# Kernel optimization log

Measured on AMD Instinct MI355X. Metric: run time of the kernel, lower is better.

Reference implementation:

```python
import jax, jax.numpy as jnp
import numpy as np

B, N, C, K1, CO = 8, 1024, 64, 3, 64  # K1 = K+1


def _prelu(x, a):
    return jnp.where(x >= 0, x, a * x)


def setup_inputs() -> dict:
    key = jax.random.key(0)
    ks = jax.random.split(key, 12)
    X_real = jax.random.normal(ks[0], (B, N, C), jnp.float32)
    X_imag = jax.random.normal(ks[1], (B, N, C), jnp.float32)
    # complex laplacian polynomial stack (B, K+1, N, N), scaled like a normalized laplacian
    L_real = jax.random.normal(ks[2], (B, K1, N, N), jnp.float32) * 0.03
    L_imag = jax.random.normal(ks[3], (B, K1, N, N), jnp.float32) * 0.03
    # Chebyshev complex weights: uniform(-stdv, stdv) then normalized to unit magnitude
    stdv = 1.0 / np.sqrt(CO)
    wr = jax.random.uniform(ks[4], (K1, C, CO), jnp.float32, -stdv, stdv)
    wi = jax.random.uniform(ks[5], (K1, C, CO), jnp.float32, -stdv, stdv)
    mag = jnp.sqrt(wr ** 2 + wi ** 2)
    w_real, w_imag = wr / mag, wi / mag
    # CVLinear(2C, 1): complex weight split into src (X_i) and dst (X_j) halves
    astd = 1.0 / np.sqrt(2 * C)
    a_src_r = jax.random.uniform(ks[6], (C,), jnp.float32, -astd, astd)
    a_src_i = jax.random.uniform(ks[7], (C,), jnp.float32, -astd, astd)
    a_dst_r = jax.random.uniform(ks[8], (C,), jnp.float32, -astd, astd)
    a_dst_i = jax.random.uniform(ks[9], (C,), jnp.float32, -astd, astd)
    attn_b_r = jax.random.uniform(ks[10], (), jnp.float32, -astd, astd)
    attn_b_i = jax.random.uniform(ks[11], (), jnp.float32, -astd, astd)
    alpha_r = jnp.float32(0.25)  # CPReLU slopes
    alpha_i = jnp.float32(0.25)
    return dict(X_real=X_real, X_imag=X_imag, L_real=L_real, L_imag=L_imag,
                a_src_r=a_src_r, a_src_i=a_src_i, a_dst_r=a_dst_r, a_dst_i=a_dst_i,
                attn_b_r=attn_b_r, attn_b_i=attn_b_i, alpha_r=alpha_r, alpha_i=alpha_i,
                w_real=w_real, w_imag=w_imag)


def reference(X_real, X_imag, L_real, L_imag, a_src_r, a_src_i, a_dst_r, a_dst_i,
              attn_b_r, attn_b_i, alpha_r, alpha_i, w_real, w_imag):
    # --- attention: complex linear over [X_i ; X_j], decomposed GAT-style ---
    # (z @ a) for complex z, a: real = zr@ar - zi@ai ; imag = zr@ai + zi@ar
    si_r = X_real @ a_src_r - X_imag @ a_src_i  # (B, N)
    si_i = X_real @ a_src_i + X_imag @ a_src_r
    sj_r = X_real @ a_dst_r - X_imag @ a_dst_i
    sj_i = X_real @ a_dst_i + X_imag @ a_dst_r
    s_r = si_r[:, :, None] + sj_r[:, None, :] + attn_b_r  # (B, N, N) scores[b,i,j]
    s_i = si_i[:, :, None] + sj_i[:, None, :] + attn_b_i
    # CPReLU: PReLU on real and imag parts independently
    s_r = _prelu(s_r, alpha_r)
    s_i = _prelu(s_i, alpha_i)
    # PhaseSoftMax(dim=1): softmax over magnitudes along axis 1, keep phase
    mag = jnp.sqrt(s_r ** 2 + s_i ** 2)
    scale = jax.nn.softmax(mag, axis=1) / jnp.maximum(mag, 1e-12)
    a_r, a_i = scale * s_r, scale * s_i  # complex attn weights (B, N, N)
    # modulate complex laplacian: L * attn (broadcast over K dim)
    Lm_r = L_real * a_r[:, None] - L_imag * a_i[:, None]  # (B, K+1, N, N)
    Lm_i = L_real * a_i[:, None] + L_imag * a_r[:, None]
    # --- Chebyshev sum: sum_k (L_k X) W_k, complex ---
    LX_r = jnp.einsum('bknm,bmc->bknc', Lm_r, X_real) - jnp.einsum('bknm,bmc->bknc', Lm_i, X_imag)
    LX_i = jnp.einsum('bknm,bmc->bknc', Lm_r, X_imag) + jnp.einsum('bknm,bmc->bknc', Lm_i, X_real)
    out_r = jnp.einsum('bknc,kco->bno', LX_r, w_real) - jnp.einsum('bknc,kco->bno', LX_i, w_imag)
    out_i = jnp.einsum('bknc,kco->bno', LX_r, w_imag) + jnp.einsum('bknc,kco->bno', LX_i, w_real)
    return jnp.stack([out_r, out_i])  # (2, B, N, C_out)
```

## Files before the change

kernel.cpp:

```cpp
#include <hip/hip_runtime.h>

typedef __attribute__((ext_vector_type(8))) short bf16x8;
typedef __attribute__((ext_vector_type(4))) float f32x4;
typedef unsigned int uint32;
typedef unsigned short u16;

#define BN 1024

__device__ __align__(16) float g_stats[6 * 8192];
__device__ __align__(16) u16   g_Xt[8 * 16 * 2 * 64 * 64];
__device__ __align__(16) u16   g_wt[6 * 64 * 192];
__device__ __align__(16) float g_part[2048 * 6144];

__device__ __forceinline__ u16 f2bf(float x) {
    uint32 u = __float_as_uint(x);
    u += 0x7fffu + ((u >> 16) & 1u);
    return (u16)(u >> 16);
}
__device__ __forceinline__ float bf2f(u16 h) {
    return __uint_as_float(((uint32)h) << 16);
}

__global__ void k_sisj(const float* __restrict__ Xr, const float* __restrict__ Xi,
                       const float* __restrict__ asr, const float* __restrict__ asi,
                       const float* __restrict__ adr, const float* __restrict__ adi) {
    int wid = threadIdx.x >> 6, lane = threadIdx.x & 63;
    int bn = blockIdx.x * 4 + wid;
    float xr = Xr[(size_t)bn * 64 + lane], xi = Xi[(size_t)bn * 64 + lane];
    float r0 = asr[lane], i0 = asi[lane], r1 = adr[lane], i1 = adi[lane];
    float v0 = xr * r0 - xi * i0;
    float v1 = xr * i0 + xi * r0;
    float v2 = xr * r1 - xi * i1;
    float v3 = xr * i1 + xi * r1;
    #pragma unroll
    for (int off = 32; off; off >>= 1) {
        v0 += __shfl_xor(v0, off);
        v1 += __shfl_xor(v1, off);
        v2 += __shfl_xor(v2, off);
        v3 += __shfl_xor(v3, off);
    }
    if (lane == 0) {
        g_stats[bn]         = v0;
        g_stats[8192 + bn]  = v1;
        g_stats[16384 + bn] = v2;
        g_stats[24576 + bn] = v3;
    }
}

__global__ void k_mz(const float* __restrict__ pbr, const float* __restrict__ pbi,
                     const float* __restrict__ par, const float* __restrict__ pai) {
    int wid = threadIdx.x >> 6, lane = threadIdx.x & 63;
    int bj = blockIdx.x * 4 + wid;
    int b = bj >> 10;
    float br = pbr[0], bi = pbi[0], ar = par[0], ai = pai[0];
    float sjrv = g_stats[16384 + bj], sjiv = g_stats[24576 + bj];
    float mags[16];
    float mx = 0.0f;
    #pragma unroll
    for (int t = 0; t < 16; ++t) {
        int i = t * 64 + lane;
        float sr = g_stats[b * BN + i] + sjrv + br;
        float si = g_stats[8192 + b * BN + i] + sjiv + bi;
        sr = sr >= 0.f ? sr : ar * sr;
        si = si >= 0.f ? si : ai * si;
        float m = sqrtf(sr * sr + si * si);
        mags[t] = m;
        mx = fmaxf(mx, m);
    }
    #pragma unroll
    for (int off = 32; off; off >>= 1) mx = fmaxf(mx, __shfl_xor(mx, off));
    float s = 0.f;
    #pragma unroll
    for (int t = 0; t < 16; ++t) s += __expf(mags[t] - mx);
    #pragma unroll
    for (int off = 32; off; off >>= 1) s += __shfl_xor(s, off);
    if (lane == 0) { g_stats[32768 + bj] = mx; g_stats[40960 + bj] = s; }
}

__global__ void k_xt(const float* __restrict__ Xr, const float* __restrict__ Xi) {
    int b = blockIdx.x >> 4, q = blockIdx.x & 15;
    __shared__ float xs[2][64][65];
    int tid = threadIdx.x;
    #pragma unroll 4
    for (int rep = 0; rep < 32; ++rep) {
        int idx = rep * 256 + tid;
        int p = idx >> 12, j = (idx >> 6) & 63, c = idx & 63;
        const float* src = p ? Xi : Xr;
        xs[p][j][c] = src[((size_t)b * BN + q * 64 + j) * 64 + c];
    }
    __syncthreads();
    #pragma unroll
    for (int rep = 0; rep < 4; ++rep) {
        int idx = rep * 256 + tid;
        int p = idx >> 9, c = (idx >> 3) & 63, j8 = idx & 7;
        union { u16 h[8]; uint4 v; } pk;
        #pragma unroll
        for (int jj = 0; jj < 8; ++jj) pk.h[jj] = f2bf(xs[p][j8 * 8 + jj][c]);
        *(uint4*)&g_Xt[(size_t)(((b * 16 + q) * 2 + p) * 64 + c) * 64 + j8 * 8] = pk.v;
    }
}

__global__ void k_wt(const float* __restrict__ wr, const float* __restrict__ wi) {
    int t = blockIdx.x * 256 + threadIdx.x;
    int o = t & 63, kc = t >> 6;
    float vr = wr[t], vi = wi[t];
    u16 rh = f2bf(vr);
    u16 rl = f2bf(vr - bf2f(rh));
    u16 ih = f2bf(vi);
    u16 il = f2bf(vi - bf2f(ih));
    g_wt[(0 * 64 + o) * 192 + kc] = rh;
    g_wt[(1 * 64 + o) * 192 + kc] = rl;
    g_wt[(2 * 64 + o) * 192 + kc] = ih;
    g_wt[(3 * 64 + o) * 192 + kc] = il;
    g_wt[(4 * 64 + o) * 192 + kc] = (u16)(ih ^ 0x8000u);
    g_wt[(5 * 64 + o) * 192 + kc] = (u16)(il ^ 0x8000u);
}

__global__ __launch_bounds__(256) void k_main(
    const float* __restrict__ Lr, const float* __restrict__ Li,
    const float* __restrict__ pbr, const float* __restrict__ pbi,
    const float* __restrict__ par, const float* __restrict__ pai) {
    __shared__ __align__(16) u16 lmS[6912];
    __shared__ __align__(16) float sA[2][16];

    int tid = threadIdx.x, wid = tid >> 6, lane = tid & 63;
    int jh = blockIdx.x & 3, it = (blockIdx.x >> 2) & 63, b = blockIdx.x >> 8;
    int i0 = it * 16;

    const float* sjr_g = g_stats + 16384;
    const float* sji_g = g_stats + 24576;
    const float* Mv_g  = g_stats + 32768;
    const float* Zv_g  = g_stats + 40960;

    if (tid < 32) {
        int p = tid >> 4, i = tid & 15;
        sA[p][i] = g_stats[p * 8192 + b * BN + i0 + i];
    }

    f32x4 zz = {0.f, 0.f, 0.f, 0.f};
    f32x4 accr[3], acci[3];
    #pragma unroll
    for (int k = 0; k < 3; ++k) { accr[k] = zz; acci[k] = zz; }

    float brv = pbr[0], biv = pbi[0], alrv = par[0], aliv = pai[0];

    int ti = tid >> 4, tj4 = tid & 15;
    int arow = lane & 15, kb = (lane >> 4) * 8;

    __syncthreads();
    float sirv = sA[0][ti], siiv = sA[1][ti];

    for (int qi = 0; qi < 4; ++qi) {
        int q = jh * 4 + qi;
        int jj0 = q * 64 + tj4 * 4;
        float4 A = *(const float4*)&sjr_g[b * BN + jj0];
        float4 Bv = *(const float4*)&sji_g[b * BN + jj0];
        float4 C = *(const float4*)&Mv_g[b * BN + jj0];
        float4 D = *(const float4*)&Zv_g[b * BN + jj0];
        float sjr4[4] = {A.x, A.y, A.z, A.w};
        float sji4[4] = {Bv.x, Bv.y, Bv.z, Bv.w};
        float M4[4]   = {C.x, C.y, C.z, C.w};
        float Z4[4]   = {D.x, D.y, D.z, D.w};
        float arj[4], aij[4];
        #pragma unroll
        for (int e = 0; e < 4; ++e) {
            float sr = sirv + sjr4[e] + brv;
            float si = siiv + sji4[e] + biv;
            sr = sr >= 0.f ? sr : alrv * sr;
            si = si >= 0.f ? si : aliv * si;
            float mg = sqrtf(sr * sr + si * si);
            float sc = __expf(mg - M4[e]) / (Z4[e] * fmaxf(mg, 1e-12f));
            arj[e] = sc * sr;
            aij[e] = sc * si;
        }
        #pragma unroll
        for (int k = 0; k < 3; ++k) {
            size_t lbase = ((size_t)(b * 3 + k) * BN + (i0 + ti)) * BN + jj0;
            float4 r4 = *(const float4*)&Lr[lbase];
            float4 s4 = *(const float4*)&Li[lbase];
            float lr4[4] = {r4.x, r4.y, r4.z, r4.w};
            float li4[4] = {s4.x, s4.y, s4.z, s4.w};
            union { u16 h[4]; uint2 v; } pr, pi;
            #pragma unroll
            for (int e = 0; e < 4; ++e) {
                float mr = lr4[e] * arj[e] - li4[e] * aij[e];
                float mi = lr4[e] * aij[e] + li4[e] * arj[e];
                pr.h[e] = f2bf(mr);
                pi.h[e] = f2bf(mi);
            }
            *(uint2*)(lmS + ((k * 2 + 0) * 16 + ti) * 72 + tj4 * 4) = pr.v;
            *(uint2*)(lmS + ((k * 2 + 1) * 16 + ti) * 72 + tj4 * 4) = pi.v;
        }
        bf16x8 Bx[2][2];
        {
            size_t xbase = (size_t)((b * 16 + q) * 2) * 4096 + (wid * 16 + arow) * 64 + kb;
            #pragma unroll
            for (int p = 0; p < 2; ++p)
                #pragma unroll
                for (int ks = 0; ks < 2; ++ks)
                    Bx[p][ks] = *(const bf16x8*)&g_Xt[xbase + p * 4096 + ks * 32];
        }
        __syncthreads();
        #pragma unroll
        for (int k = 0; k < 3; ++k) {
            #pragma unroll
            for (int ks = 0; ks < 2; ++ks) {
                int kc = ks * 32 + kb;
                bf16x8 aR = *(const bf16x8*)(lmS + ((k * 2 + 0) * 16 + arow) * 72 + kc);
                bf16x8 aI = *(const bf16x8*)(lmS + ((k * 2 + 1) * 16 + arow) * 72 + kc);
                bf16x8 aIn;
                #pragma unroll
                for (int z = 0; z < 8; ++z) aIn[z] = (short)(aI[z] ^ (short)0x8000);
                accr[k] = __builtin_amdgcn_mfma_f32_16x16x32_bf16(aR,  Bx[0][ks], accr[k], 0, 0, 0);
                accr[k] = __builtin_amdgcn_mfma_f32_16x16x32_bf16(aIn, Bx[1][ks], accr[k], 0, 0, 0);
                acci[k] = __builtin_amdgcn_mfma_f32_16x16x32_bf16(aR,  Bx[1][ks], acci[k], 0, 0, 0);
                acci[k] = __builtin_amdgcn_mfma_f32_16x16x32_bf16(aI,  Bx[0][ks], acci[k], 0, 0, 0);
            }
        }
        __syncthreads();
    }

    {
        size_t base = (size_t)blockIdx.x * 6144;
        #pragma unroll
        for (int k = 0; k < 3; ++k) {
            #pragma unroll
            for (int p = 0; p < 2; ++p) {
                f32x4 fr = p ? acci[k] : accr[k];
                #pragma unroll
                for (int r = 0; r < 4; ++r) {
                    int row = (lane >> 4) * 4 + r;
                    int kc = k * 64 + wid * 16 + (lane & 15);
                    g_part[base + (size_t)(p * 16 + row) * 192 + kc] = fr[r];
                }
            }
        }
    }
}

__global__ __launch_bounds__(256) void k_out(float* __restrict__ out) {
    __shared__ __align__(16) u16 LXs[12800];
    int tid = threadIdx.x, wid = tid >> 6, lane = tid & 63;
    int b = blockIdx.x >> 6, it = blockIdx.x & 63, i0 = it * 16;
    size_t p0 = (size_t)((b * 64 + it) * 4) * 6144;

    #pragma unroll
    for (int rep = 0; rep < 6; ++rep) {
        int idx = rep * 256 + tid;
        float4 a0 = *(const float4*)&g_part[p0 + (size_t)idx * 4];
        float4 a1 = *(const float4*)&g_part[p0 + 6144 + (size_t)idx * 4];
        float4 a2 = *(const float4*)&g_part[p0 + 12288 + (size_t)idx * 4];
        float4 a3 = *(const float4*)&g_part[p0 + 18432 + (size_t)idx * 4];
        float s[4] = {a0.x + a1.x + a2.x + a3.x, a0.y + a1.y + a2.y + a3.y,
                      a0.z + a1.z + a2.z + a3.z, a0.w + a1.w + a2.w + a3.w};
        int f0 = idx * 4;
        int rc = f0 / 3072, rem = f0 - rc * 3072;
        int row = rem / 192, kc = rem - row * 192;
        #pragma unroll
        for (int t = 0; t < 4; ++t) {
            float v = s[t];
            u16 hi = f2bf(v);
            u16 lo = f2bf(v - bf2f(hi));
            LXs[((rc * 2 + 0) * 16 + row) * 200 + kc + t] = hi;
            LXs[((rc * 2 + 1) * 16 + row) * 200 + kc + t] = lo;
        }
    }
    __syncthreads();

    f32x4 zz = {0.f, 0.f, 0.f, 0.f};
    f32x4 o_r = zz, o_i = zz;
    int arow = lane & 15, kb = (lane >> 4) * 8;
    int o = wid * 16 + arow;
    #pragma unroll
    for (int ks = 0; ks < 6; ++ks) {
        int kc = ks * 32 + kb;
        bf16x8 Arh = *(const bf16x8*)(LXs + (0 * 16 + arow) * 200 + kc);
        bf16x8 Arl = *(const bf16x8*)(LXs + (1 * 16 + arow) * 200 + kc);
        bf16x8 Aih = *(const bf16x8*)(LXs + (2 * 16 + arow) * 200 + kc);
        bf16x8 Ail = *(const bf16x8*)(LXs + (3 * 16 + arow) * 200 + kc);
        bf16x8 Wrh  = *(const bf16x8*)&g_wt[(0 * 64 + o) * 192 + kc];
        bf16x8 Wrl  = *(const bf16x8*)&g_wt[(1 * 64 + o) * 192 + kc];
        bf16x8 Wih  = *(const bf16x8*)&g_wt[(2 * 64 + o) * 192 + kc];
        bf16x8 Wil  = *(const bf16x8*)&g_wt[(3 * 64 + o) * 192 + kc];
        bf16x8 Wihn = *(const bf16x8*)&g_wt[(4 * 64 + o) * 192 + kc];
        bf16x8 Wiln = *(const bf16x8*)&g_wt[(5 * 64 + o) * 192 + kc];
        o_r = __builtin_amdgcn_mfma_f32_16x16x32_bf16(Arh, Wrh,  o_r, 0, 0, 0);
        o_r = __builtin_amdgcn_mfma_f32_16x16x32_bf16(Arh, Wrl,  o_r, 0, 0, 0);
        o_r = __builtin_amdgcn_mfma_f32_16x16x32_bf16(Arl, Wrh,  o_r, 0, 0, 0);
        o_r = __builtin_amdgcn_mfma_f32_16x16x32_bf16(Aih, Wihn, o_r, 0, 0, 0);
        o_r = __builtin_amdgcn_mfma_f32_16x16x32_bf16(Aih, Wiln, o_r, 0, 0, 0);
        o_r = __builtin_amdgcn_mfma_f32_16x16x32_bf16(Ail, Wihn, o_r, 0, 0, 0);
        o_i = __builtin_amdgcn_mfma_f32_16x16x32_bf16(Arh, Wih,  o_i, 0, 0, 0);
        o_i = __builtin_amdgcn_mfma_f32_16x16x32_bf16(Arh, Wil,  o_i, 0, 0, 0);
        o_i = __builtin_amdgcn_mfma_f32_16x16x32_bf16(Arl, Wih,  o_i, 0, 0, 0);
        o_i = __builtin_amdgcn_mfma_f32_16x16x32_bf16(Aih, Wrh,  o_i, 0, 0, 0);
        o_i = __builtin_amdgcn_mfma_f32_16x16x32_bf16(Aih, Wrl,  o_i, 0, 0, 0);
        o_i = __builtin_amdgcn_mfma_f32_16x16x32_bf16(Ail, Wrh,  o_i, 0, 0, 0);
    }
    #pragma unroll
    for (int r = 0; r < 4; ++r) {
        int i = (lane >> 4) * 4 + r;
        size_t off = ((size_t)b * BN + i0 + i) * 64 + o;
        out[off] = o_r[r];
        out[524288 + off] = o_i[r];
    }
}

extern "C" void kernel_launch(void* const* d_in, const int* in_sizes, int n_in,
                              void* d_out, int out_size, void* d_ws, size_t ws_size,
                              hipStream_t stream) {
    const float* Xr  = (const float*)d_in[0];
    const float* Xi  = (const float*)d_in[1];
    const float* Lr  = (const float*)d_in[2];
    const float* Li  = (const float*)d_in[3];
    const float* asr = (const float*)d_in[4];
    const float* asi = (const float*)d_in[5];
    const float* adr = (const float*)d_in[6];
    const float* adi = (const float*)d_in[7];
    const float* pbr = (const float*)d_in[8];
    const float* pbi = (const float*)d_in[9];
    const float* par = (const float*)d_in[10];
    const float* pai = (const float*)d_in[11];
    const float* wr  = (const float*)d_in[12];
    const float* wi  = (const float*)d_in[13];
    float* out = (float*)d_out;

    k_sisj<<<2048, 256, 0, stream>>>(Xr, Xi, asr, asi, adr, adi);
    k_mz<<<2048, 256, 0, stream>>>(pbr, pbi, par, pai);
    k_xt<<<128, 256, 0, stream>>>(Xr, Xi);
    k_wt<<<48, 256, 0, stream>>>(wr, wi);
    k_main<<<2048, 256, 0, stream>>>(Lr, Li, pbr, pbi, par, pai);
    k_out<<<512, 256, 0, stream>>>(out);
}
```

Before: 87.33 us.

## Double k_main row tile to 32 rows and stage column stats in LDS

k_main now handles 32 rows per block instead of 16, which halves the grid and gives each wave two row-group MFMA accumulators. Each block's B-operand X fragments are reused across twice as many rows, and the per-column softmax stats are preloaded once into shared memory instead of being re-read from global memory every iteration. Each thread now loads 8 L elements per row as two float4 loads and writes 16-byte LDS stores. The partial-sum layout and k_out indexing are adjusted to match. In exchange, LDS use and register pressure per block rise and the grid has fewer blocks.

```diff
diff --git a/kernel.cpp b/kernel.cpp
--- a/kernel.cpp
+++ b/kernel.cpp
@@ -10,7 +10,7 @@
 __device__ __align__(16) float g_stats[6 * 8192];
 __device__ __align__(16) u16   g_Xt[8 * 16 * 2 * 64 * 64];
 __device__ __align__(16) u16   g_wt[6 * 64 * 192];
-__device__ __align__(16) float g_part[2048 * 6144];
+__device__ __align__(16) float g_part[1024 * 12288];
 
 __device__ __forceinline__ u16 f2bf(float x) {
     uint32 u = __float_as_uint(x);
@@ -120,31 +120,36 @@
     const float* __restrict__ Lr, const float* __restrict__ Li,
     const float* __restrict__ pbr, const float* __restrict__ pbi,
     const float* __restrict__ par, const float* __restrict__ pai) {
-    __shared__ __align__(16) u16 lmS[6912];
-    __shared__ __align__(16) float sA[2][16];
+    __shared__ __align__(16) u16 lmS[13824];
+    __shared__ __align__(16) float stS[4][256];
+    __shared__ __align__(16) float sA[2][32];
 
     int tid = threadIdx.x, wid = tid >> 6, lane = tid & 63;
-    int jh = blockIdx.x & 3, it = (blockIdx.x >> 2) & 63, b = blockIdx.x >> 8;
-    int i0 = it * 16;
-
-    const float* sjr_g = g_stats + 16384;
-    const float* sji_g = g_stats + 24576;
-    const float* Mv_g  = g_stats + 32768;
-    const float* Zv_g  = g_stats + 40960;
-
-    if (tid < 32) {
-        int p = tid >> 4, i = tid & 15;
-        sA[p][i] = g_stats[p * 8192 + b * BN + i0 + i];
+    int jh = blockIdx.x & 3, it = (blockIdx.x >> 2) & 31, b = blockIdx.x >> 7;
+    int i0 = it * 32;
+
+    {
+        int jg = b * BN + jh * 256 + tid;
+        stS[0][tid] = g_stats[16384 + jg];
+        stS[1][tid] = g_stats[24576 + jg];
+        stS[2][tid] = g_stats[32768 + jg];
+        stS[3][tid] = g_stats[40960 + jg];
+        if (tid < 64) {
+            int p = tid >> 5, i = tid & 31;
+            sA[p][i] = g_stats[p * 8192 + b * BN + i0 + i];
+        }
     }
 
     f32x4 zz = {0.f, 0.f, 0.f, 0.f};
-    f32x4 accr[3], acci[3];
-    #pragma unroll
-    for (int k = 0; k < 3; ++k) { accr[k] = zz; acci[k] = zz; }
+    f32x4 accr[3][2], acci[3][2];
+    #pragma unroll
+    for (int k = 0; k < 3; ++k)
+        #pragma unroll
+        for (int g = 0; g < 2; ++g) { accr[k][g] = zz; acci[k][g] = zz; }
 
     float brv = pbr[0], biv = pbi[0], alrv = par[0], aliv = pai[0];
 
-    int ti = tid >> 4, tj4 = tid & 15;
+    int ti = tid >> 3, tj8 = tid & 7;
     int arow = lane & 15, kb = (lane >> 4) * 8;
 
     __syncthreads();
@@ -152,44 +157,36 @@
 
     for (int qi = 0; qi < 4; ++qi) {
         int q = jh * 4 + qi;
-        int jj0 = q * 64 + tj4 * 4;
-        float4 A = *(const float4*)&sjr_g[b * BN + jj0];
-        float4 Bv = *(const float4*)&sji_g[b * BN + jj0];
-        float4 C = *(const float4*)&Mv_g[b * BN + jj0];
-        float4 D = *(const float4*)&Zv_g[b * BN + jj0];
-        float sjr4[4] = {A.x, A.y, A.z, A.w};
-        float sji4[4] = {Bv.x, Bv.y, Bv.z, Bv.w};
-        float M4[4]   = {C.x, C.y, C.z, C.w};
-        float Z4[4]   = {D.x, D.y, D.z, D.w};
-        float arj[4], aij[4];
-        #pragma unroll
-        for (int e = 0; e < 4; ++e) {
-            float sr = sirv + sjr4[e] + brv;
-            float si = siiv + sji4[e] + biv;
+        int jloc = qi * 64 + tj8 * 8;
+        float arj[8], aij[8];
+        #pragma unroll
+        for (int e = 0; e < 8; ++e) {
+            float sr = sirv + stS[0][jloc + e] + brv;
+            float si = siiv + stS[1][jloc + e] + biv;
             sr = sr >= 0.f ? sr : alrv * sr;
             si = si >= 0.f ? si : aliv * si;
             float mg = sqrtf(sr * sr + si * si);
-            float sc = __expf(mg - M4[e]) / (Z4[e] * fmaxf(mg, 1e-12f));
+            float sc = __expf(mg - stS[2][jloc + e]) / (stS[3][jloc + e] * fmaxf(mg, 1e-12f));
             arj[e] = sc * sr;
             aij[e] = sc * si;
         }
         #pragma unroll
         for (int k = 0; k < 3; ++k) {
-            size_t lbase = ((size_t)(b * 3 + k) * BN + (i0 + ti)) * BN + jj0;
-            float4 r4 = *(const float4*)&Lr[lbase];
-            float4 s4 = *(const float4*)&Li[lbase];
-            float lr4[4] = {r4.x, r4.y, r4.z, r4.w};
-            float li4[4] = {s4.x, s4.y, s4.z, s4.w};
-            union { u16 h[4]; uint2 v; } pr, pi;
+            size_t lbase = ((size_t)(b * 3 + k) * BN + (i0 + ti)) * BN + q * 64 + tj8 * 8;
+            float4 r0 = *(const float4*)&Lr[lbase], r1 = *(const float4*)&Lr[lbase + 4];
+            float4 s0 = *(const float4*)&Li[lbase], s1 = *(const float4*)&Li[lbase + 4];
+            float lr8[8] = {r0.x, r0.y, r0.z, r0.w, r1.x, r1.y, r1.z, r1.w};
+            float li8[8] = {s0.x, s0.y, s0.z, s0.w, s1.x, s1.y, s1.z, s1.w};
+            union { u16 h[8]; uint4 v; } pr, pi;
             #pragma unroll
-            for (int e = 0; e < 4; ++e) {
-                float mr = lr4[e] * arj[e] - li4[e] * aij[e];
-                float mi = lr4[e] * aij[e] + li4[e] * arj[e];
+            for (int e = 0; e < 8; ++e) {
+                float mr = lr8[e] * arj[e] - li8[e] * aij[e];
+                float mi = lr8[e] * aij[e] + li8[e] * arj[e];
                 pr.h[e] = f2bf(mr);
                 pi.h[e] = f2bf(mi);
             }
-            *(uint2*)(lmS + ((k * 2 + 0) * 16 + ti) * 72 + tj4 * 4) = pr.v;
-            *(uint2*)(lmS + ((k * 2 + 1) * 16 + ti) * 72 + tj4 * 4) = pi.v;
+            *(uint4*)(lmS + ((k * 2 + 0) * 32 + ti) * 72 + tj8 * 8) = pr.v;
+            *(uint4*)(lmS + ((k * 2 + 1) * 32 + ti) * 72 + tj8 * 8) = pi.v;
         }
         bf16x8 Bx[2][2];
         {
@@ -206,32 +203,38 @@
             #pragma unroll
             for (int ks = 0; ks < 2; ++ks) {
                 int kc = ks * 32 + kb;
-                bf16x8 aR = *(const bf16x8*)(lmS + ((k * 2 + 0) * 16 + arow) * 72 + kc);
-                bf16x8 aI = *(const bf16x8*)(lmS + ((k * 2 + 1) * 16 + arow) * 72 + kc);
-                bf16x8 aIn;
                 #pragma unroll
-                for (int z = 0; z < 8; ++z) aIn[z] = (short)(aI[z] ^ (short)0x8000);
-                accr[k] = __builtin_amdgcn_mfma_f32_16x16x32_bf16(aR,  Bx[0][ks], accr[k], 0, 0, 0);
-                accr[k] = __builtin_amdgcn_mfma_f32_16x16x32_bf16(aIn, Bx[1][ks], accr[k], 0, 0, 0);
-                acci[k] = __builtin_amdgcn_mfma_f32_16x16x32_bf16(aR,  Bx[1][ks], acci[k], 0, 0, 0);
-                acci[k] = __builtin_amdgcn_mfma_f32_16x16x32_bf16(aI,  Bx[0][ks], acci[k], 0, 0, 0);
+                for (int g = 0; g < 2; ++g) {
+                    bf16x8 aR = *(const bf16x8*)(lmS + ((k * 2 + 0) * 32 + g * 16 + arow) * 72 + kc);
+                    bf16x8 aI = *(const bf16x8*)(lmS + ((k * 2 + 1) * 32 + g * 16 + arow) * 72 + kc);
+                    bf16x8 aIn;
+                    #pragma unroll
+                    for (int z = 0; z < 8; ++z) aIn[z] = (short)(aI[z] ^ (short)0x8000);
+                    accr[k][g] = __builtin_amdgcn_mfma_f32_16x16x32_bf16(aR,  Bx[0][ks], accr[k][g], 0, 0, 0);
+                    accr[k][g] = __builtin_amdgcn_mfma_f32_16x16x32_bf16(aIn, Bx[1][ks], accr[k][g], 0, 0, 0);
+                    acci[k][g] = __builtin_amdgcn_mfma_f32_16x16x32_bf16(aR,  Bx[1][ks], acci[k][g], 0, 0, 0);
+                    acci[k][g] = __builtin_amdgcn_mfma_f32_16x16x32_bf16(aI,  Bx[0][ks], acci[k][g], 0, 0, 0);
+                }
             }
         }
         __syncthreads();
     }
 
     {
-        size_t base = (size_t)blockIdx.x * 6144;
+        size_t base = (size_t)blockIdx.x * 12288;
         #pragma unroll
         for (int k = 0; k < 3; ++k) {
+            int kc = k * 64 + wid * 16 + arow;
             #pragma unroll
-            for (int p = 0; p < 2; ++p) {
-                f32x4 fr = p ? acci[k] : accr[k];
+            for (int g = 0; g < 2; ++g) {
                 #pragma unroll
-                for (int r = 0; r < 4; ++r) {
-                    int row = (lane >> 4) * 4 + r;
-                    int kc = k * 64 + wid * 16 + (lane & 15);
-                    g_part[base + (size_t)(p * 16 + row) * 192 + kc] = fr[r];
+                for (int p = 0; p < 2; ++p) {
+                    f32x4 fr = p ? acci[k][g] : accr[k][g];
+                    #pragma unroll
+                    for (int r = 0; r < 4; ++r) {
+                        int row = g * 16 + (lane >> 4) * 4 + r;
+                        g_part[base + (size_t)(p * 32 + row) * 192 + kc] = fr[r];
+                    }
                 }
             }
         }
@@ -241,21 +244,23 @@
 __global__ __launch_bounds__(256) void k_out(float* __restrict__ out) {
     __shared__ __align__(16) u16 LXs[12800];
     int tid = threadIdx.x, wid = tid >> 6, lane = tid & 63;
-    int b = blockIdx.x >> 6, it = blockIdx.x & 63, i0 = it * 16;
-    size_t p0 = (size_t)((b * 64 + it) * 4) * 6144;
+    int b = blockIdx.x >> 6, it16 = blockIdx.x & 63, i0 = it16 * 16;
+    int it32 = it16 >> 1, rowoff = (it16 & 1) * 16;
+    size_t pb = (size_t)((b * 32 + it32) * 4) * 12288;
 
     #pragma unroll
     for (int rep = 0; rep < 6; ++rep) {
         int idx = rep * 256 + tid;
-        float4 a0 = *(const float4*)&g_part[p0 + (size_t)idx * 4];
-        float4 a1 = *(const float4*)&g_part[p0 + 6144 + (size_t)idx * 4];
-        float4 a2 = *(const float4*)&g_part[p0 + 12288 + (size_t)idx * 4];
-        float4 a3 = *(const float4*)&g_part[p0 + 18432 + (size_t)idx * 4];
-        float s[4] = {a0.x + a1.x + a2.x + a3.x, a0.y + a1.y + a2.y + a3.y,
-                      a0.z + a1.z + a2.z + a3.z, a0.w + a1.w + a2.w + a3.w};
         int f0 = idx * 4;
         int rc = f0 / 3072, rem = f0 - rc * 3072;
         int row = rem / 192, kc = rem - row * 192;
+        size_t off = (size_t)(rc * 32 + rowoff + row) * 192 + kc;
+        float4 a0 = *(const float4*)&g_part[pb + off];
+        float4 a1 = *(const float4*)&g_part[pb + 12288 + off];
+        float4 a2 = *(const float4*)&g_part[pb + 24576 + off];
+        float4 a3 = *(const float4*)&g_part[pb + 36864 + off];
+        float s[4] = {a0.x + a1.x + a2.x + a3.x, a0.y + a1.y + a2.y + a3.y,
+                      a0.z + a1.z + a2.z + a3.z, a0.w + a1.w + a2.w + a3.w};
         #pragma unroll
         for (int t = 0; t < 4; ++t) {
             float v = s[t];
@@ -329,6 +334,6 @@
     k_mz<<<2048, 256, 0, stream>>>(pbr, pbi, par, pai);
     k_xt<<<128, 256, 0, stream>>>(Xr, Xi);
     k_wt<<<48, 256, 0, stream>>>(wr, wi);
-    k_main<<<2048, 256, 0, stream>>>(Lr, Li, pbr, pbi, par, pai);
+    k_main<<<1024, 256, 0, stream>>>(Lr, Li, pbr, pbi, par, pai);
     k_out<<<512, 256, 0, stream>>>(out);
 }
```

After: 98.13 us. 1.12x slower.

## Double-buffer Laplacian tiles via async global-to-LDS loads and halve j-split

Applied to the files above, without the earlier changes.

The main kernel now streams the L_real/L_imag tiles straight into a double-buffered shared-memory region with global_load_lds, prefetching the next 64-column chunk while the current one is processed. Explicit vmcnt waits and raw barriers replace __syncthreads. Per-column softmax stats are cached once in LDS instead of being reloaded each iteration, and each block now covers 512 columns instead of 256. That halves the block count and the partial-sum traffic that k_out must reduce. The trade-off is much higher LDS use per block and lower occupancy and grid parallelism, and the hand-tuned waitcnt values are fragile.

```diff
diff --git a/kernel.cpp b/kernel.cpp
--- a/kernel.cpp
+++ b/kernel.cpp
@@ -10,7 +10,7 @@
 __device__ __align__(16) float g_stats[6 * 8192];
 __device__ __align__(16) u16   g_Xt[8 * 16 * 2 * 64 * 64];
 __device__ __align__(16) u16   g_wt[6 * 64 * 192];
-__device__ __align__(16) float g_part[2048 * 6144];
+__device__ __align__(16) float g_part[1024 * 6144];
 
 __device__ __forceinline__ u16 f2bf(float x) {
     uint32 u = __float_as_uint(x);
@@ -19,6 +19,11 @@
 }
 __device__ __forceinline__ float bf2f(u16 h) {
     return __uint_as_float(((uint32)h) << 16);
+}
+__device__ __forceinline__ void gl_lds16(const float* g, float* l) {
+    __builtin_amdgcn_global_load_lds(
+        (const __attribute__((address_space(1))) uint32*)g,
+        (__attribute__((address_space(3))) uint32*)l, 16, 0, 0);
 }
 
 __global__ void k_sisj(const float* __restrict__ Xr, const float* __restrict__ Xi,
@@ -120,64 +125,95 @@
     const float* __restrict__ Lr, const float* __restrict__ Li,
     const float* __restrict__ pbr, const float* __restrict__ pbi,
     const float* __restrict__ par, const float* __restrict__ pai) {
+    __shared__ __align__(16) float Lbuf[2][6144];
     __shared__ __align__(16) u16 lmS[6912];
+    __shared__ __align__(16) float stS[4][512];
     __shared__ __align__(16) float sA[2][16];
 
-    int tid = threadIdx.x, wid = tid >> 6, lane = tid & 63;
-    int jh = blockIdx.x & 3, it = (blockIdx.x >> 2) & 63, b = blockIdx.x >> 8;
+    int tid = threadIdx.x, w = tid >> 6, lane = tid & 63;
+    int jh = blockIdx.x & 1, it = (blockIdx.x >> 1) & 63, b = blockIdx.x >> 7;
     int i0 = it * 16;
-
-    const float* sjr_g = g_stats + 16384;
-    const float* sji_g = g_stats + 24576;
-    const float* Mv_g  = g_stats + 32768;
-    const float* Zv_g  = g_stats + 40960;
-
-    if (tid < 32) {
-        int p = tid >> 4, i = tid & 15;
-        sA[p][i] = g_stats[p * 8192 + b * BN + i0 + i];
-    }
+    int arow = lane & 15, kb = (lane >> 4) * 8;
+    int ti = tid >> 4, tj4 = tid & 15;
+
+    {
+        int jg = b * BN + jh * 512 + tid;
+        stS[0][tid] = g_stats[16384 + jg];
+        stS[1][tid] = g_stats[24576 + jg];
+        stS[2][tid] = g_stats[32768 + jg];
+        stS[3][tid] = g_stats[40960 + jg];
+        stS[0][tid + 256] = g_stats[16384 + jg + 256];
+        stS[1][tid + 256] = g_stats[24576 + jg + 256];
+        stS[2][tid + 256] = g_stats[32768 + jg + 256];
+        stS[3][tid + 256] = g_stats[40960 + jg + 256];
+        if (tid < 32) {
+            int p = tid >> 4, i = tid & 15;
+            sA[p][i] = g_stats[p * 8192 + b * BN + i0 + i];
+        }
+    }
+    __syncthreads();
+
+    float brv = pbr[0], biv = pbi[0], alrv = par[0], aliv = pai[0];
+    float sirv = sA[0][ti], siiv = sA[1][ti];
 
     f32x4 zz = {0.f, 0.f, 0.f, 0.f};
     f32x4 accr[3], acci[3];
     #pragma unroll
     for (int k = 0; k < 3; ++k) { accr[k] = zz; acci[k] = zz; }
 
-    float brv = pbr[0], biv = pbi[0], alrv = par[0], aliv = pai[0];
-
-    int ti = tid >> 4, tj4 = tid & 15;
-    int arow = lane & 15, kb = (lane >> 4) * 8;
-
-    __syncthreads();
-    float sirv = sA[0][ti], siiv = sA[1][ti];
-
-    for (int qi = 0; qi < 4; ++qi) {
-        int q = jh * 4 + qi;
-        int jj0 = q * 64 + tj4 * 4;
-        float4 A = *(const float4*)&sjr_g[b * BN + jj0];
-        float4 Bv = *(const float4*)&sji_g[b * BN + jj0];
-        float4 C = *(const float4*)&Mv_g[b * BN + jj0];
-        float4 D = *(const float4*)&Zv_g[b * BN + jj0];
-        float sjr4[4] = {A.x, A.y, A.z, A.w};
-        float sji4[4] = {Bv.x, Bv.y, Bv.z, Bv.w};
-        float M4[4]   = {C.x, C.y, C.z, C.w};
-        float Z4[4]   = {D.x, D.y, D.z, D.w};
+    auto stageL = [&](int q, int buf) {
+        #pragma unroll
+        for (int t = 0; t < 6; ++t) {
+            int l = w * 6 + t;
+            int k = l >> 3, rc = (l >> 2) & 1, rg = l & 3;
+            int row = rg * 4 + (lane >> 4), j = (lane & 15) * 4;
+            const float* src = rc ? Li : Lr;
+            const float* g = src + ((size_t)(b * 3 + k) * BN + (i0 + row)) * BN
+                                 + jh * 512 + q * 64 + j;
+            gl_lds16(g, &Lbuf[buf][l * 256]);
+        }
+    };
+
+    stageL(0, 0);
+
+    #pragma unroll
+    for (int qi = 0; qi < 8; ++qi) {
+        int q = jh * 8 + qi;
+        int cur = qi & 1;
+        bf16x8 Bxr[2], Bxi_[2];
+        {
+            size_t xb = (size_t)((b * 16 + q) * 2) * 4096 + (size_t)(w * 16 + arow) * 64 + kb;
+            #pragma unroll
+            for (int ks = 0; ks < 2; ++ks) {
+                Bxr[ks]  = *(const bf16x8*)&g_Xt[xb + ks * 32];
+                Bxi_[ks] = *(const bf16x8*)&g_Xt[xb + 4096 + ks * 32];
+            }
+        }
+        if (qi < 7) stageL(qi + 1, cur ^ 1);
         float arj[4], aij[4];
-        #pragma unroll
-        for (int e = 0; e < 4; ++e) {
-            float sr = sirv + sjr4[e] + brv;
-            float si = siiv + sji4[e] + biv;
-            sr = sr >= 0.f ? sr : alrv * sr;
-            si = si >= 0.f ? si : aliv * si;
-            float mg = sqrtf(sr * sr + si * si);
-            float sc = __expf(mg - M4[e]) / (Z4[e] * fmaxf(mg, 1e-12f));
-            arj[e] = sc * sr;
-            aij[e] = sc * si;
-        }
+        {
+            int jloc = qi * 64 + tj4 * 4;
+            #pragma unroll
+            for (int e = 0; e < 4; ++e) {
+                float sr = sirv + stS[0][jloc + e] + brv;
+                float si = siiv + stS[1][jloc + e] + biv;
+                sr = sr >= 0.f ? sr : alrv * sr;
+                si = si >= 0.f ? si : aliv * si;
+                float mg = sqrtf(sr * sr + si * si);
+                float sc = __expf(mg - stS[2][jloc + e]) / (stS[3][jloc + e] * fmaxf(mg, 1e-12f));
+                arj[e] = sc * sr;
+                aij[e] = sc * si;
+            }
+        }
+        if (qi < 7) { asm volatile("s_waitcnt vmcnt(10)" ::: "memory"); }
+        else        { asm volatile("s_waitcnt vmcnt(4)"  ::: "memory"); }
+        __builtin_amdgcn_s_barrier();
+        __builtin_amdgcn_sched_barrier(0);
         #pragma unroll
         for (int k = 0; k < 3; ++k) {
-            size_t lbase = ((size_t)(b * 3 + k) * BN + (i0 + ti)) * BN + jj0;
-            float4 r4 = *(const float4*)&Lr[lbase];
-            float4 s4 = *(const float4*)&Li[lbase];
+            int base = (k * 8 + (ti >> 2)) * 256 + (ti & 3) * 64 + tj4 * 4;
+            float4 r4 = *(const float4*)&Lbuf[cur][base];
+            float4 s4 = *(const float4*)&Lbuf[cur][base + 1024];
             float lr4[4] = {r4.x, r4.y, r4.z, r4.w};
             float li4[4] = {s4.x, s4.y, s4.z, s4.w};
             union { u16 h[4]; uint2 v; } pr, pi;
@@ -191,16 +227,9 @@
             *(uint2*)(lmS + ((k * 2 + 0) * 16 + ti) * 72 + tj4 * 4) = pr.v;
             *(uint2*)(lmS + ((k * 2 + 1) * 16 + ti) * 72 + tj4 * 4) = pi.v;
         }
-        bf16x8 Bx[2][2];
-        {
-            size_t xbase = (size_t)((b * 16 + q) * 2) * 4096 + (wid * 16 + arow) * 64 + kb;
-            #pragma unroll
-            for (int p = 0; p < 2; ++p)
-                #pragma unroll
-                for (int ks = 0; ks < 2; ++ks)
-                    Bx[p][ks] = *(const bf16x8*)&g_Xt[xbase + p * 4096 + ks * 32];
-        }
-        __syncthreads();
+        asm volatile("s_waitcnt lgkmcnt(0)" ::: "memory");
+        __builtin_amdgcn_s_barrier();
+        __builtin_amdgcn_sched_barrier(0);
         #pragma unroll
         for (int k = 0; k < 3; ++k) {
             #pragma unroll
@@ -211,26 +240,29 @@
                 bf16x8 aIn;
                 #pragma unroll
                 for (int z = 0; z < 8; ++z) aIn[z] = (short)(aI[z] ^ (short)0x8000);
-                accr[k] = __builtin_amdgcn_mfma_f32_16x16x32_bf16(aR,  Bx[0][ks], accr[k], 0, 0, 0);
-                accr[k] = __builtin_amdgcn_mfma_f32_16x16x32_bf16(aIn, Bx[1][ks], accr[k], 0, 0, 0);
-                acci[k] = __builtin_amdgcn_mfma_f32_16x16x32_bf16(aR,  Bx[1][ks], acci[k], 0, 0, 0);
-                acci[k] = __builtin_amdgcn_mfma_f32_16x16x32_bf16(aI,  Bx[0][ks], acci[k], 0, 0, 0);
-            }
-        }
-        __syncthreads();
+                accr[k] = __builtin_amdgcn_mfma_f32_16x16x32_bf16(aR,  Bxr[ks],  accr[k], 0, 0, 0);
+                acci[k] = __builtin_amdgcn_mfma_f32_16x16x32_bf16(aR,  Bxi_[ks], acci[k], 0, 0, 0);
+                acci[k] = __builtin_amdgcn_mfma_f32_16x16x32_bf16(aI,  Bxr[ks],  acci[k], 0, 0, 0);
+                #pragma unroll
+                for (int z = 0; z < 8; ++z) aIn[z] = (short)(aIn[z]);
+                accr[k] = __builtin_amdgcn_mfma_f32_16x16x32_bf16(aIn, Bxi_[ks], accr[k], 0, 0, 0);
+            }
+        }
+        asm volatile("s_waitcnt lgkmcnt(0)" ::: "memory");
+        __builtin_amdgcn_s_barrier();
     }
 
     {
         size_t base = (size_t)blockIdx.x * 6144;
         #pragma unroll
         for (int k = 0; k < 3; ++k) {
+            int kc = k * 64 + w * 16 + arow;
             #pragma unroll
             for (int p = 0; p < 2; ++p) {
                 f32x4 fr = p ? acci[k] : accr[k];
                 #pragma unroll
                 for (int r = 0; r < 4; ++r) {
                     int row = (lane >> 4) * 4 + r;
-                    int kc = k * 64 + wid * 16 + (lane & 15);
                     g_part[base + (size_t)(p * 16 + row) * 192 + kc] = fr[r];
                 }
             }
@@ -242,17 +274,15 @@
     __shared__ __align__(16) u16 LXs[12800];
     int tid = threadIdx.x, wid = tid >> 6, lane = tid & 63;
     int b = blockIdx.x >> 6, it = blockIdx.x & 63, i0 = it * 16;
-    size_t p0 = (size_t)((b * 64 + it) * 4) * 6144;
+    size_t p0 = (size_t)((b * 64 + it) * 2 + 0) * 6144;
+    size_t p1 = p0 + 6144;
 
     #pragma unroll
     for (int rep = 0; rep < 6; ++rep) {
         int idx = rep * 256 + tid;
-        float4 a0 = *(const float4*)&g_part[p0 + (size_t)idx * 4];
-        float4 a1 = *(const float4*)&g_part[p0 + 6144 + (size_t)idx * 4];
-        float4 a2 = *(const float4*)&g_part[p0 + 12288 + (size_t)idx * 4];
-        float4 a3 = *(const float4*)&g_part[p0 + 18432 + (size_t)idx * 4];
-        float s[4] = {a0.x + a1.x + a2.x + a3.x, a0.y + a1.y + a2.y + a3.y,
-                      a0.z + a1.z + a2.z + a3.z, a0.w + a1.w + a2.w + a3.w};
+        float4 a = *(const float4*)&g_part[p0 + (size_t)idx * 4];
+        float4 c = *(const float4*)&g_part[p1 + (size_t)idx * 4];
+        float s[4] = {a.x + c.x, a.y + c.y, a.z + c.z, a.w + c.w};
         int f0 = idx * 4;
         int rc = f0 / 3072, rem = f0 - rc * 3072;
         int row = rem / 192, kc = rem - row * 192;
@@ -329,6 +359,6 @@
     k_mz<<<2048, 256, 0, stream>>>(pbr, pbi, par, pai);
     k_xt<<<128, 256, 0, stream>>>(Xr, Xi);
     k_wt<<<48, 256, 0, stream>>>(wr, wi);
-    k_main<<<2048, 256, 0, stream>>>(Lr, Li, pbr, pbi, par, pai);
+    k_main<<<1024, 256, 0, stream>>>(Lr, Li, pbr, pbi, par, pai);
     k_out<<<512, 256, 0, stream>>>(out);
 }
```

After: 82.23 us. -5.8%, faster.

## Stage full 256-column L tile in LDS once, then run all MFMAs

Applied to the files above, without the earlier changes.

Instead of four iterations that each load a 64-column slice of L, modulate it, sync twice and run MFMAs, the kernel now stages the j-range statistics in shared memory, loads and modulates the whole 16x256 slab for all three k in one phase, and then runs all eight MFMA steps after a single barrier. Each thread now handles 4 rows x 4 columns with coalesced 1KB row reads, and the negation moves from the A operand to the X operand. The aim is fewer barriers and more memory loads in flight, at the cost of much larger LDS use (about 50KB), which may lower occupancy and leaves no overlap between the load and MFMA phases.

```diff
diff --git a/kernel.cpp b/kernel.cpp
--- a/kernel.cpp
+++ b/kernel.cpp
@@ -120,117 +120,118 @@
     const float* __restrict__ Lr, const float* __restrict__ Li,
     const float* __restrict__ pbr, const float* __restrict__ pbi,
     const float* __restrict__ par, const float* __restrict__ pai) {
-    __shared__ __align__(16) u16 lmS[6912];
+    __shared__ __align__(16) u16 lmS[25344];
+    __shared__ __align__(16) float stS[4][256];
     __shared__ __align__(16) float sA[2][16];
 
-    int tid = threadIdx.x, wid = tid >> 6, lane = tid & 63;
+    int tid = threadIdx.x, w = tid >> 6, lane = tid & 63;
     int jh = blockIdx.x & 3, it = (blockIdx.x >> 2) & 63, b = blockIdx.x >> 8;
-    int i0 = it * 16;
-
-    const float* sjr_g = g_stats + 16384;
-    const float* sji_g = g_stats + 24576;
-    const float* Mv_g  = g_stats + 32768;
-    const float* Zv_g  = g_stats + 40960;
-
-    if (tid < 32) {
-        int p = tid >> 4, i = tid & 15;
-        sA[p][i] = g_stats[p * 8192 + b * BN + i0 + i];
-    }
+    int i0 = it * 16, j0 = jh * 256;
+
+    {
+        int jg = b * BN + j0 + tid;
+        stS[0][tid] = g_stats[16384 + jg];
+        stS[1][tid] = g_stats[24576 + jg];
+        stS[2][tid] = g_stats[32768 + jg];
+        stS[3][tid] = g_stats[40960 + jg];
+        if (tid < 32) {
+            int p = tid >> 4, i = tid & 15;
+            sA[p][i] = g_stats[p * 8192 + b * BN + i0 + i];
+        }
+    }
+    __syncthreads();
+
+    float brv = pbr[0], biv = pbi[0], alrv = par[0], aliv = pai[0];
+
+    {
+        float4 s0 = *(const float4*)&stS[0][lane * 4];
+        float4 s1 = *(const float4*)&stS[1][lane * 4];
+        float4 s2 = *(const float4*)&stS[2][lane * 4];
+        float4 s3 = *(const float4*)&stS[3][lane * 4];
+        float sjr4[4] = {s0.x, s0.y, s0.z, s0.w};
+        float sji4[4] = {s1.x, s1.y, s1.z, s1.w};
+        float M4[4]   = {s2.x, s2.y, s2.z, s2.w};
+        float Z4[4]   = {s3.x, s3.y, s3.z, s3.w};
+        float arj[4][4], aij[4][4];
+        #pragma unroll
+        for (int u = 0; u < 4; ++u) {
+            int row = w * 4 + u;
+            float sirv = sA[0][row], siiv = sA[1][row];
+            #pragma unroll
+            for (int e = 0; e < 4; ++e) {
+                float sr = sirv + sjr4[e] + brv;
+                float si = siiv + sji4[e] + biv;
+                sr = sr >= 0.f ? sr : alrv * sr;
+                si = si >= 0.f ? si : aliv * si;
+                float mg = sqrtf(sr * sr + si * si);
+                float sc = __expf(mg - M4[e]) / (Z4[e] * fmaxf(mg, 1e-12f));
+                arj[u][e] = sc * sr;
+                aij[u][e] = sc * si;
+            }
+        }
+        #pragma unroll
+        for (int k = 0; k < 3; ++k) {
+            #pragma unroll
+            for (int u = 0; u < 4; ++u) {
+                int row = w * 4 + u;
+                size_t gb = ((size_t)(b * 3 + k) * BN + (i0 + row)) * BN + j0 + lane * 4;
+                float4 r4 = *(const float4*)&Lr[gb];
+                float4 s4 = *(const float4*)&Li[gb];
+                float lr4[4] = {r4.x, r4.y, r4.z, r4.w};
+                float li4[4] = {s4.x, s4.y, s4.z, s4.w};
+                union { u16 h[4]; uint2 v; } pr, pi;
+                #pragma unroll
+                for (int e = 0; e < 4; ++e) {
+                    float mr = lr4[e] * arj[u][e] - li4[e] * aij[u][e];
+                    float mi = lr4[e] * aij[u][e] + li4[e] * arj[u][e];
+                    pr.h[e] = f2bf(mr);
+                    pi.h[e] = f2bf(mi);
+                }
+                *(uint2*)(lmS + ((k * 2 + 0) * 16 + row) * 264 + lane * 4) = pr.v;
+                *(uint2*)(lmS + ((k * 2 + 1) * 16 + row) * 264 + lane * 4) = pi.v;
+            }
+        }
+    }
+    __syncthreads();
 
     f32x4 zz = {0.f, 0.f, 0.f, 0.f};
     f32x4 accr[3], acci[3];
     #pragma unroll
     for (int k = 0; k < 3; ++k) { accr[k] = zz; acci[k] = zz; }
-
-    float brv = pbr[0], biv = pbi[0], alrv = par[0], aliv = pai[0];
-
-    int ti = tid >> 4, tj4 = tid & 15;
     int arow = lane & 15, kb = (lane >> 4) * 8;
 
-    __syncthreads();
-    float sirv = sA[0][ti], siiv = sA[1][ti];
-
-    for (int qi = 0; qi < 4; ++qi) {
-        int q = jh * 4 + qi;
-        int jj0 = q * 64 + tj4 * 4;
-        float4 A = *(const float4*)&sjr_g[b * BN + jj0];
-        float4 Bv = *(const float4*)&sji_g[b * BN + jj0];
-        float4 C = *(const float4*)&Mv_g[b * BN + jj0];
-        float4 D = *(const float4*)&Zv_g[b * BN + jj0];
-        float sjr4[4] = {A.x, A.y, A.z, A.w};
-        float sji4[4] = {Bv.x, Bv.y, Bv.z, Bv.w};
-        float M4[4]   = {C.x, C.y, C.z, C.w};
-        float Z4[4]   = {D.x, D.y, D.z, D.w};
-        float arj[4], aij[4];
-        #pragma unroll
-        for (int e = 0; e < 4; ++e) {
-            float sr = sirv + sjr4[e] + brv;
-            float si = siiv + sji4[e] + biv;
-            sr = sr >= 0.f ? sr : alrv * sr;
-            si = si >= 0.f ? si : aliv * si;
-            float mg = sqrtf(sr * sr + si * si);
-            float sc = __expf(mg - M4[e]) / (Z4[e] * fmaxf(mg, 1e-12f));
-            arj[e] = sc * sr;
-            aij[e] = sc * si;
-        }
+    #pragma unroll
+    for (int s = 0; s < 8; ++s) {
+        int q = jh * 4 + (s >> 1);
+        int jin = (s & 1) * 32;
+        size_t xb = (size_t)((b * 16 + q) * 2) * 4096 + (size_t)(w * 16 + arow) * 64 + jin + kb;
+        bf16x8 Bxr = *(const bf16x8*)&g_Xt[xb];
+        bf16x8 Bxi = *(const bf16x8*)&g_Xt[xb + 4096];
+        bf16x8 nBxi;
+        #pragma unroll
+        for (int z = 0; z < 8; ++z) nBxi[z] = (short)(Bxi[z] ^ (short)0x8000);
         #pragma unroll
         for (int k = 0; k < 3; ++k) {
-            size_t lbase = ((size_t)(b * 3 + k) * BN + (i0 + ti)) * BN + jj0;
-            float4 r4 = *(const float4*)&Lr[lbase];
-            float4 s4 = *(const float4*)&Li[lbase];
-            float lr4[4] = {r4.x, r4.y, r4.z, r4.w};
-            float li4[4] = {s4.x, s4.y, s4.z, s4.w};
-            union { u16 h[4]; uint2 v; } pr, pi;
-            #pragma unroll
-            for (int e = 0; e < 4; ++e) {
-                float mr = lr4[e] * arj[e] - li4[e] * aij[e];
-                float mi = lr4[e] * aij[e] + li4[e] * arj[e];
-                pr.h[e] = f2bf(mr);
-                pi.h[e] = f2bf(mi);
-            }
-            *(uint2*)(lmS + ((k * 2 + 0) * 16 + ti) * 72 + tj4 * 4) = pr.v;
-            *(uint2*)(lmS + ((k * 2 + 1) * 16 + ti) * 72 + tj4 * 4) = pi.v;
-        }
-        bf16x8 Bx[2][2];
-        {
-            size_t xbase = (size_t)((b * 16 + q) * 2) * 4096 + (wid * 16 + arow) * 64 + kb;
-            #pragma unroll
-            for (int p = 0; p < 2; ++p)
-                #pragma unroll
-                for (int ks = 0; ks < 2; ++ks)
-                    Bx[p][ks] = *(const bf16x8*)&g_Xt[xbase + p * 4096 + ks * 32];
-        }
-        __syncthreads();
-        #pragma unroll
-        for (int k = 0; k < 3; ++k) {
-            #pragma unroll
-            for (int ks = 0; ks < 2; ++ks) {
-                int kc = ks * 32 + kb;
-                bf16x8 aR = *(const bf16x8*)(lmS + ((k * 2 + 0) * 16 + arow) * 72 + kc);
-                bf16x8 aI = *(const bf16x8*)(lmS + ((k * 2 + 1) * 16 + arow) * 72 + kc);
-                bf16x8 aIn;
-                #pragma unroll
-                for (int z = 0; z < 8; ++z) aIn[z] = (short)(aI[z] ^ (short)0x8000);
-                accr[k] = __builtin_amdgcn_mfma_f32_16x16x32_bf16(aR,  Bx[0][ks], accr[k], 0, 0, 0);
-                accr[k] = __builtin_amdgcn_mfma_f32_16x16x32_bf16(aIn, Bx[1][ks], accr[k], 0, 0, 0);
-                acci[k] = __builtin_amdgcn_mfma_f32_16x16x32_bf16(aR,  Bx[1][ks], acci[k], 0, 0, 0);
-                acci[k] = __builtin_amdgcn_mfma_f32_16x16x32_bf16(aI,  Bx[0][ks], acci[k], 0, 0, 0);
-            }
-        }
-        __syncthreads();
+            bf16x8 aR = *(const bf16x8*)(lmS + ((k * 2 + 0) * 16 + arow) * 264 + s * 32 + kb);
+            bf16x8 aI = *(const bf16x8*)(lmS + ((k * 2 + 1) * 16 + arow) * 264 + s * 32 + kb);
+            accr[k] = __builtin_amdgcn_mfma_f32_16x16x32_bf16(aR, Bxr,  accr[k], 0, 0, 0);
+            accr[k] = __builtin_amdgcn_mfma_f32_16x16x32_bf16(aI, nBxi, accr[k], 0, 0, 0);
+            acci[k] = __builtin_amdgcn_mfma_f32_16x16x32_bf16(aR, Bxi,  acci[k], 0, 0, 0);
+            acci[k] = __builtin_amdgcn_mfma_f32_16x16x32_bf16(aI, Bxr,  acci[k], 0, 0, 0);
+        }
     }
 
     {
         size_t base = (size_t)blockIdx.x * 6144;
         #pragma unroll
         for (int k = 0; k < 3; ++k) {
+            int kc = k * 64 + w * 16 + arow;
             #pragma unroll
             for (int p = 0; p < 2; ++p) {
                 f32x4 fr = p ? acci[k] : accr[k];
                 #pragma unroll
                 for (int r = 0; r < 4; ++r) {
                     int row = (lane >> 4) * 4 + r;
-                    int kc = k * 64 + wid * 16 + (lane & 15);
                     g_part[base + (size_t)(p * 16 + row) * 192 + kc] = fr[r];
                 }
             }
```

Result: slower. 99.89 us (+14.4%).
